# Optimization experiments

Hardware: AMD Instinct MI355X
Metric: run time of the kernel (lower is better)

Reference implementation:

```python
import jax, jax.numpy as jnp
import numpy as np

D_MODEL = 1024
HEADS = 16
D_K = D_MODEL // HEADS
B, S = 4, 2048


def setup_inputs() -> dict:
    key = jax.random.key(0)
    ks = jax.random.split(key, 12)
    xav = float(np.sqrt(6.0 / (D_MODEL + D_MODEL)))  # xavier_uniform bound
    inp = {
        "query": jax.random.normal(ks[0], (B, S, D_MODEL), jnp.float32),
        "key": jax.random.normal(ks[1], (B, S, D_MODEL), jnp.float32),
        "value": jax.random.normal(ks[2], (B, S, D_MODEL), jnp.float32),
        # causal mask, broadcast over batch and heads: [1,1,S,S]
        "mask": jnp.tril(jnp.ones((S, S), jnp.int32))[None, None],
        "Wq": jax.random.uniform(ks[3], (D_MODEL, D_MODEL), jnp.float32, -xav, xav),
        "bq": jnp.zeros((D_MODEL,), jnp.float32),
        "Wk": jax.random.uniform(ks[4], (D_MODEL, D_MODEL), jnp.float32, -xav, xav),
        "bk": jnp.zeros((D_MODEL,), jnp.float32),
        "Wv": jax.random.uniform(ks[5], (D_MODEL, D_MODEL), jnp.float32, -xav, xav),
        "bv": jnp.zeros((D_MODEL,), jnp.float32),
        "Wo": jax.random.uniform(ks[6], (D_MODEL, D_MODEL), jnp.float32, -xav, xav),
        "bo": jnp.zeros((D_MODEL,), jnp.float32),
    }
    return inp


def reference(query, key, value, mask, Wq, bq, Wk, bk, Wv, bv, Wo, bo):
    b, s, d = query.shape
    # torch Linear: y = x @ W.T + b, W is [out, in]
    Q = (jnp.einsum("bsd,ed->bse", query, Wq) + bq).reshape(b, s, HEADS, D_K).transpose(0, 2, 1, 3)
    K = (jnp.einsum("bsd,ed->bse", key, Wk) + bk).reshape(b, -1, HEADS, D_K).transpose(0, 2, 1, 3)
    V = (jnp.einsum("bsd,ed->bse", value, Wv) + bv).reshape(b, -1, HEADS, D_K).transpose(0, 2, 1, 3)
    scale = 1.0 / jnp.sqrt(jnp.asarray(D_K, query.dtype))
    scores = jnp.einsum("bhqd,bhkd->bhqk", Q, K) * scale  # [B,H,S,S]
    scores = jnp.where(mask == 0, -jnp.inf, scores)
    attn = jax.nn.softmax(scores, axis=-1)
    attn = jnp.where(jnp.isnan(attn), jnp.zeros_like(attn), attn)  # nan-fix as in source
    out = jnp.einsum("bhqk,bhkd->bhqd", attn, V)
    out = out.transpose(0, 2, 1, 3).reshape(b, s, d)
    return jnp.einsum("bsd,ed->bse", out, Wo) + bo
```

## Files before the change

kernel.cpp:

```cpp
#include <hip/hip_runtime.h>
#include <hip/hip_bf16.h>

#define DM 1024
#define NHEADS 16
#define DKH 64
#define BATCH 4
#define SEQ 2048
#define MROWS (BATCH*SEQ)

typedef __attribute__((ext_vector_type(8))) short bf16x8;
typedef __attribute__((ext_vector_type(4))) short bf16x4;
typedef __attribute__((ext_vector_type(4))) float f32x4;

#if __has_builtin(__builtin_amdgcn_exp2f)
#define EXP2(x) __builtin_amdgcn_exp2f(x)
#else
#define EXP2(x) exp2f(x)
#endif

__device__ __forceinline__ unsigned short f2bf(float f){
  unsigned u = __float_as_uint(f);
  u += 0x7fffu + ((u >> 16) & 1u);
  return (unsigned short)(u >> 16);
}

__device__ __forceinline__ unsigned pk2bf(float lo, float hi){
  union { __hip_bfloat162 h; unsigned u; } c;
  c.h = __float22bfloat162_rn(make_float2(lo, hi));
  return c.u;
}

__device__ __forceinline__ bf16x8 cvtA8(float4 a, float4 b){
  union { unsigned u[4]; bf16x8 v; } r;
  r.u[0] = pk2bf(a.x, a.y);
  r.u[1] = pk2bf(a.z, a.w);
  r.u[2] = pk2bf(b.x, b.y);
  r.u[3] = pk2bf(b.z, b.w);
  return r.v;
}

__device__ __forceinline__ void gload16(const unsigned short* g, unsigned short* l){
  __builtin_amdgcn_global_load_lds((const __attribute__((address_space(1))) void*)g,
                                   (__attribute__((address_space(3))) void*)l, 16, 0, 0);
}

struct ConvArgs { const float* src[4]; unsigned short* dst[4]; };

__global__ __launch_bounds__(256) void conv_w(ConvArgs a){
  const int t = blockIdx.x >> 10;
  const int boff = blockIdx.x & 1023;
  const float* __restrict__ src = a.src[t];
  unsigned short* __restrict__ dst = a.dst[t];
  const int i = (boff * 256 + threadIdx.x) * 4;
  const float4 v = *reinterpret_cast<const float4*>(src + i);
  ushort4 o;
  o.x = f2bf(v.x); o.y = f2bf(v.y); o.z = f2bf(v.z); o.w = f2bf(v.w);
  *reinterpret_cast<ushort4*>(dst + i) = o;
}

template<int MODE, int AFP32>
__global__ __launch_bounds__(256)
void gemm_bt(const void* __restrict__ Av, const unsigned short* __restrict__ Bw,
             const float* __restrict__ bias, void* __restrict__ out, float scale)
{
  const int K = 1024;
  __shared__ short a_sh[128*64];
  __shared__ short b_sh[128*64];
  const int tid  = threadIdx.x;
  const int lane = tid & 63;
  const int wid  = tid >> 6;
  const int wm = wid >> 1, wn = wid & 1;
  const int lin = blockIdx.x;
  const int xcd = lin & 7;
  const int i9  = lin >> 3;
  const int tileM = (8*xcd + (i9 >> 3)) * 128;
  const int tileN = (i9 & 7) * 128;

  f32x4 acc[4][4];
  #pragma unroll
  for (int i = 0; i < 4; i++)
    #pragma unroll
    for (int j = 0; j < 4; j++)
      acc[i][j] = (f32x4){0.f,0.f,0.f,0.f};

  const int lr = lane & 15;
  const int lg = lane >> 4;

  const int r8 = lane >> 3, c8 = lane & 7;
  const int srow = 8*wid + r8;
  const int sgrp = (c8 ^ r8) * 8;

  for (int k0 = 0; k0 < K; k0 += 64){
    bf16x8 ra[4];
    if constexpr (AFP32){
      const float* Af = (const float*)Av;
      #pragma unroll
      for (int i = 0; i < 4; i++){
        int v   = tid + 256*i;
        int row = v >> 3;
        int cg  = v & 7;
        const float4 f0 = *reinterpret_cast<const float4*>(Af + (size_t)(tileM+row)*K + k0 + cg*8);
        const float4 f1 = *reinterpret_cast<const float4*>(Af + (size_t)(tileM+row)*K + k0 + cg*8 + 4);
        ra[i] = cvtA8(f0, f1);
      }
    }
    __syncthreads();
    #pragma unroll
    for (int j = 0; j < 4; j++){
      gload16(Bw + (size_t)(tileN + srow + 32*j)*K + k0 + sgrp,
              (unsigned short*)&b_sh[(8*wid + 32*j)*64]);
    }
    if constexpr (AFP32){
      #pragma unroll
      for (int i = 0; i < 4; i++){
        int v   = tid + 256*i;
        int row = v >> 3;
        int cg  = v & 7;
        *reinterpret_cast<bf16x8*>(&a_sh[row*64 + ((cg ^ (row & 7)) * 8)]) = ra[i];
      }
    } else {
      const unsigned short* Ab = (const unsigned short*)Av;
      #pragma unroll
      for (int j = 0; j < 4; j++){
        gload16(Ab + (size_t)(tileM + srow + 32*j)*K + k0 + sgrp,
                (unsigned short*)&a_sh[(8*wid + 32*j)*64]);
      }
    }
    __syncthreads();

    #pragma unroll
    for (int kk = 0; kk < 64; kk += 32){
      bf16x8 af[4], bfr[4];
      const int g0 = lg + (kk >> 3);
      #pragma unroll
      for (int fm = 0; fm < 4; fm++){
        int row = wm*64 + fm*16 + lr;
        af[fm] = *reinterpret_cast<const bf16x8*>(&a_sh[row*64 + ((g0 ^ (row & 7)) * 8)]);
      }
      #pragma unroll
      for (int fn = 0; fn < 4; fn++){
        int row = wn*64 + fn*16 + lr;
        bfr[fn] = *reinterpret_cast<const bf16x8*>(&b_sh[row*64 + ((g0 ^ (row & 7)) * 8)]);
      }
      #pragma unroll
      for (int fm = 0; fm < 4; fm++)
        #pragma unroll
        for (int fn = 0; fn < 4; fn++)
          acc[fm][fn] = __builtin_amdgcn_mfma_f32_16x16x32_bf16(af[fm], bfr[fn], acc[fm][fn], 0, 0, 0);
    }
  }

  #pragma unroll
  for (int fm = 0; fm < 4; fm++){
    #pragma unroll
    for (int fn = 0; fn < 4; fn++){
      #pragma unroll
      for (int r = 0; r < 4; r++){
        int m = tileM + wm*64 + fm*16 + lg*4 + r;
        int n = tileN + wn*64 + fn*16 + lr;
        float val = acc[fm][fn][r] + bias[n];
        if (MODE == 0){
          val *= scale;
          int b = m >> 11, s = m & 2047, h = n >> 6, d = n & 63;
          ((unsigned short*)out)[(((size_t)(b*NHEADS + h)*SEQ + s)*DKH + d)] = f2bf(val);
        } else if (MODE == 1){
          int b = m >> 11, s = m & 2047, h = n >> 6, d = n & 63;
          ((unsigned short*)out)[(((size_t)(b*NHEADS + h)*DKH + d)*SEQ + s)] = f2bf(val);
        } else {
          ((float*)out)[(size_t)m*DM + n] = val;
        }
      }
    }
  }
}

__global__ __launch_bounds__(256, 4)
void attn_kernel(const unsigned short* __restrict__ Q, const unsigned short* __restrict__ Kb,
                 const unsigned short* __restrict__ Vt, unsigned short* __restrict__ Oout)
{
  __shared__ unsigned short k_sh[2][64*64];
  __shared__ unsigned short v_sh[2][64*64];
  const int lane = threadIdx.x & 63;
  const int w    = threadIdx.x >> 6;
  const int lr = lane & 15, grp = lane >> 4;
  const int bh = blockIdx.x;
  const int qtile = 15 - (int)blockIdx.y;
  const int qb0 = qtile * 128;
  const int qw0 = qb0 + w * 32;
  const int b = bh >> 4, h = bh & 15;
  const size_t kbase = (size_t)bh * SEQ * DKH;
  const size_t vbase = (size_t)bh * DKH * SEQ;

  const int r8 = lane >> 3, c8 = lane & 7;
  const int rowS0 = w*16 + r8;
  const int rowS1 = w*16 + 8 + r8;
  const size_t offK0 = (size_t)rowS0*DKH  + (size_t)((c8 ^ (rowS0 & 7)) * 8);
  const size_t offK1 = (size_t)rowS1*DKH  + (size_t)((c8 ^ (rowS1 & 7)) * 8);
  const size_t offV0 = (size_t)rowS0*SEQ  + (size_t)((c8 ^ (rowS0 & 7)) * 8);
  const size_t offV1 = (size_t)rowS1*SEQ  + (size_t)((c8 ^ (rowS1 & 7)) * 8);
  const int ldsA = (w*16)*64;
  const int ldsB = (w*16+8)*64;

  bf16x8 qf[2][2];
  #pragma unroll
  for (int qg = 0; qg < 2; qg++){
    size_t off = kbase + (size_t)(qw0 + qg*16 + lr)*DKH + grp*8;
    qf[qg][0] = *reinterpret_cast<const bf16x8*>(Q + off);
    qf[qg][1] = *reinterpret_cast<const bf16x8*>(Q + off + 32);
  }

  bf16x4 ones4;
  ones4[0] = (short)0x3F80; ones4[1] = (short)0x3F80;
  ones4[2] = (short)0x3F80; ones4[3] = (short)0x3F80;

  float mrun[2] = {-__builtin_inff(), -__builtin_inff()};
  f32x4 ls[2];
  f32x4 o[2][4];
  #pragma unroll
  for (int qg = 0; qg < 2; qg++){
    ls[qg] = (f32x4){0.f,0.f,0.f,0.f};
    #pragma unroll
    for (int dc = 0; dc < 4; dc++) o[qg][dc] = (f32x4){0.f,0.f,0.f,0.f};
  }

  const int nkb = qb0/64 + 2;

#define STAGE(kb_, bf_) do { \
    gload16(Kb + kbase + (size_t)(kb_)*4096 + offK0, (unsigned short*)&k_sh[bf_][ldsA]); \
    gload16(Kb + kbase + (size_t)(kb_)*4096 + offK1, (unsigned short*)&k_sh[bf_][ldsB]); \
    gload16(Vt + vbase + (size_t)(kb_)*64   + offV0, (unsigned short*)&v_sh[bf_][ldsA]); \
    gload16(Vt + vbase + (size_t)(kb_)*64   + offV1, (unsigned short*)&v_sh[bf_][ldsB]); \
  } while(0)

  STAGE(0, 0);
  __syncthreads();

  for (int kb = 0; kb < nkb; kb++){
    const int buf = kb & 1;
    if (kb + 1 < nkb) STAGE(kb + 1, buf ^ 1);

    if (kb*64 <= qw0 + 31){
      const unsigned short* ks = k_sh[buf];
      const unsigned short* vs = v_sh[buf];
      const bool act0 = (kb*64 <= qw0 + 15);

      bf16x4 pb[2][4];
      #pragma unroll
      for (int qg = 0; qg < 2; qg++){
        if (qg == 0 && !act0) continue;
        f32x4 st[4];
        __builtin_amdgcn_s_setprio(1);
        #pragma unroll
        for (int ksub = 0; ksub < 4; ksub++){
          int rowk = ksub*16 + lr;
          bf16x8 kf0 = *reinterpret_cast<const bf16x8*>(&ks[rowk*64 + ((grp ^ (rowk & 7)) * 8)]);
          bf16x8 kf1 = *reinterpret_cast<const bf16x8*>(&ks[rowk*64 + (((4 + grp) ^ (rowk & 7)) * 8)]);
          f32x4 s = (f32x4){0.f,0.f,0.f,0.f};
          s = __builtin_amdgcn_mfma_f32_16x16x32_bf16(kf0, qf[qg][0], s, 0, 0, 0);
          s = __builtin_amdgcn_mfma_f32_16x16x32_bf16(kf1, qf[qg][1], s, 0, 0, 0);
          st[ksub] = s;
        }
        __builtin_amdgcn_s_setprio(0);

        const int qgb = qw0 + qg*16;
        if (kb*64 + 63 > qgb){
          #pragma unroll
          for (int ksub = 0; ksub < 4; ksub++)
            #pragma unroll
            for (int r = 0; r < 4; r++){
              int kg = kb*64 + ksub*16 + grp*4 + r;
              if (kg > qgb + lr) st[ksub][r] = -__builtin_inff();
            }
        }
        float mt = fmaxf(fmaxf(st[0][0], st[0][1]), fmaxf(st[0][2], st[0][3]));
        #pragma unroll
        for (int ksub = 1; ksub < 4; ksub++){
          mt = fmaxf(mt, fmaxf(fmaxf(st[ksub][0], st[ksub][1]),
                               fmaxf(st[ksub][2], st[ksub][3])));
        }
        mt = fmaxf(mt, __shfl_xor(mt, 16));
        mt = fmaxf(mt, __shfl_xor(mt, 32));
        const float mnew = fmaxf(mrun[qg], mt);
        const float corr = EXP2(mrun[qg] - mnew);
        mrun[qg] = mnew;
        #pragma unroll
        for (int dc = 0; dc < 4; dc++){
          o[qg][dc][0] *= corr; o[qg][dc][1] *= corr;
          o[qg][dc][2] *= corr; o[qg][dc][3] *= corr;
        }
        ls[qg][0] *= corr;
        #pragma unroll
        for (int ksub = 0; ksub < 4; ksub++){
          float p0 = EXP2(st[ksub][0] - mnew);
          float p1 = EXP2(st[ksub][1] - mnew);
          float p2 = EXP2(st[ksub][2] - mnew);
          float p3 = EXP2(st[ksub][3] - mnew);
          union { unsigned u[2]; bf16x4 v; } pk;
          pk.u[0] = pk2bf(p0, p1);
          pk.u[1] = pk2bf(p2, p3);
          pb[qg][ksub] = pk.v;
        }
      }

      __builtin_amdgcn_s_setprio(1);
      #pragma unroll
      for (int ksub = 0; ksub < 4; ksub++){
        #pragma unroll
        for (int dc = 0; dc < 4; dc++){
          int rowd = dc*16 + lr;
          int cg16 = ksub*2 + (grp >> 1);
          bf16x4 vf = *reinterpret_cast<const bf16x4*>(
              &vs[rowd*64 + ((cg16 ^ (rowd & 7)) * 8) + (grp & 1)*4]);
          if (act0) o[0][dc] = __builtin_amdgcn_mfma_f32_16x16x16bf16_1k(vf, pb[0][ksub], o[0][dc], 0, 0, 0);
          o[1][dc] = __builtin_amdgcn_mfma_f32_16x16x16bf16_1k(vf, pb[1][ksub], o[1][dc], 0, 0, 0);
        }
        if (act0) ls[0] = __builtin_amdgcn_mfma_f32_16x16x16bf16_1k(ones4, pb[0][ksub], ls[0], 0, 0, 0);
        ls[1] = __builtin_amdgcn_mfma_f32_16x16x16bf16_1k(ones4, pb[1][ksub], ls[1], 0, 0, 0);
      }
      __builtin_amdgcn_s_setprio(0);
    }
    __syncthreads();
  }
#undef STAGE

  #pragma unroll
  for (int qg = 0; qg < 2; qg++){
    float inv = 1.0f / ls[qg][0];
    int qglob = qw0 + qg*16 + lr;
    size_t ob = ((size_t)(b*SEQ + qglob))*DM + h*DKH;
    #pragma unroll
    for (int dc = 0; dc < 4; dc++){
      ushort4 pk;
      pk.x = f2bf(o[qg][dc][0]*inv);
      pk.y = f2bf(o[qg][dc][1]*inv);
      pk.z = f2bf(o[qg][dc][2]*inv);
      pk.w = f2bf(o[qg][dc][3]*inv);
      *reinterpret_cast<ushort4*>(&Oout[ob + dc*16 + grp*4]) = pk;
    }
  }
}

extern "C" void kernel_launch(void* const* d_in, const int* in_sizes, int n_in,
                              void* d_out, int out_size, void* d_ws, size_t ws_size,
                              hipStream_t stream) {
  const float* query = (const float*)d_in[0];
  const float* key   = (const float*)d_in[1];
  const float* value = (const float*)d_in[2];
  const float* Wq = (const float*)d_in[4];
  const float* bq = (const float*)d_in[5];
  const float* Wk = (const float*)d_in[6];
  const float* bk = (const float*)d_in[7];
  const float* Wv = (const float*)d_in[8];
  const float* bv = (const float*)d_in[9];
  const float* Wo = (const float*)d_in[10];
  const float* bo = (const float*)d_in[11];
  float* out = (float*)d_out;

  char* ws = (char*)d_ws;
  const size_t SZ_X = (size_t)MROWS * DM * 2;
  const size_t SZ_W = (size_t)DM * DM * 2;
  unsigned short* wqb = (unsigned short*)(ws + 0);
  unsigned short* wkb = (unsigned short*)(ws + SZ_W);
  unsigned short* wvb = (unsigned short*)(ws + 2*SZ_W);
  unsigned short* wob = (unsigned short*)(ws + 3*SZ_W);
  unsigned short* Qb   = (unsigned short*)(ws + 4*SZ_W);
  unsigned short* Kbuf = (unsigned short*)(ws + 4*SZ_W + SZ_X);
  unsigned short* Vt   = (unsigned short*)(ws + 4*SZ_W + 2*SZ_X);
  unsigned short* attO = (unsigned short*)(ws + 4*SZ_W + 3*SZ_X);

  ConvArgs ca;
  ca.src[0] = Wq; ca.src[1] = Wk; ca.src[2] = Wv; ca.src[3] = Wo;
  ca.dst[0] = wqb; ca.dst[1] = wkb; ca.dst[2] = wvb; ca.dst[3] = wob;
  conv_w<<<4096, 256, 0, stream>>>(ca);

  const int NBLK = (MROWS/128) * (DM/128);
  const float qscale = 0.125f * 1.4426950408889634f;
  gemm_bt<1,1><<<NBLK, 256, 0, stream>>>(value, wvb, bv, (void*)Vt,   1.0f);
  gemm_bt<0,1><<<NBLK, 256, 0, stream>>>(query, wqb, bq, (void*)Qb,   qscale);
  gemm_bt<0,1><<<NBLK, 256, 0, stream>>>(key,   wkb, bk, (void*)Kbuf, 1.0f);

  attn_kernel<<<dim3(64, 16), 256, 0, stream>>>(Qb, Kbuf, Vt, attO);

  gemm_bt<2,0><<<NBLK, 256, 0, stream>>>(attO, wob, bo, (void*)out, 1.0f);
}
```

Baseline: 198.6 us.

## Batch Q/K/V projections into one launch and rebalance causal attention tile order

The three separate projection GEMM launches become one grid of 1536 blocks that selects its input, weight, bias and output layout per block, removing two launches and the tail idle time between them. The output projection becomes its own specialized kernel with the bf16 A path only. The attention kernel's query-tile mapping changes from strictly descending order to an interleaved order that mixes heavy and light causal tiles, to even out load across CUs. This adds a runtime branch on the block index in the epilogue.

```diff
diff --git a/kernel.cpp b/kernel.cpp
--- a/kernel.cpp
+++ b/kernel.cpp
@@ -58,10 +58,123 @@
   *reinterpret_cast<ushort4*>(dst + i) = o;
 }
 
-template<int MODE, int AFP32>
+struct QKVArgs {
+  const float* A[3];
+  const unsigned short* W[3];
+  const float* bias[3];
+  unsigned short* out[3];
+  float scale[3];
+};
+
 __global__ __launch_bounds__(256)
-void gemm_bt(const void* __restrict__ Av, const unsigned short* __restrict__ Bw,
-             const float* __restrict__ bias, void* __restrict__ out, float scale)
+void gemm_qkv(QKVArgs args)
+{
+  const int K = 1024;
+  __shared__ short a_sh[128*64];
+  __shared__ short b_sh[128*64];
+  const int tid  = threadIdx.x;
+  const int lane = tid & 63;
+  const int wid  = tid >> 6;
+  const int wm = wid >> 1, wn = wid & 1;
+  const int z   = blockIdx.x >> 9;
+  const int lin = blockIdx.x & 511;
+  const int xcd = lin & 7;
+  const int i9  = lin >> 3;
+  const int tileM = (8*xcd + (i9 >> 3)) * 128;
+  const int tileN = (i9 & 7) * 128;
+
+  const float* __restrict__ Af = args.A[z];
+  const unsigned short* __restrict__ Bw = args.W[z];
+  const float* __restrict__ bias = args.bias[z];
+  unsigned short* __restrict__ outp = args.out[z];
+  const float scale = args.scale[z];
+
+  f32x4 acc[4][4];
+  #pragma unroll
+  for (int i = 0; i < 4; i++)
+    #pragma unroll
+    for (int j = 0; j < 4; j++)
+      acc[i][j] = (f32x4){0.f,0.f,0.f,0.f};
+
+  const int lr = lane & 15;
+  const int lg = lane >> 4;
+
+  const int r8 = lane >> 3, c8 = lane & 7;
+  const int srow = 8*wid + r8;
+  const int sgrp = (c8 ^ r8) * 8;
+
+  for (int k0 = 0; k0 < K; k0 += 64){
+    bf16x8 ra[4];
+    #pragma unroll
+    for (int i = 0; i < 4; i++){
+      int v   = tid + 256*i;
+      int row = v >> 3;
+      int cg  = v & 7;
+      const float4 f0 = *reinterpret_cast<const float4*>(Af + (size_t)(tileM+row)*K + k0 + cg*8);
+      const float4 f1 = *reinterpret_cast<const float4*>(Af + (size_t)(tileM+row)*K + k0 + cg*8 + 4);
+      ra[i] = cvtA8(f0, f1);
+    }
+    __syncthreads();
+    #pragma unroll
+    for (int j = 0; j < 4; j++){
+      gload16(Bw + (size_t)(tileN + srow + 32*j)*K + k0 + sgrp,
+              (unsigned short*)&b_sh[(8*wid + 32*j)*64]);
+    }
+    #pragma unroll
+    for (int i = 0; i < 4; i++){
+      int v   = tid + 256*i;
+      int row = v >> 3;
+      int cg  = v & 7;
+      *reinterpret_cast<bf16x8*>(&a_sh[row*64 + ((cg ^ (row & 7)) * 8)]) = ra[i];
+    }
+    __syncthreads();
+
+    #pragma unroll
+    for (int kk = 0; kk < 64; kk += 32){
+      bf16x8 af[4], bfr[4];
+      const int g0 = lg + (kk >> 3);
+      #pragma unroll
+      for (int fm = 0; fm < 4; fm++){
+        int row = wm*64 + fm*16 + lr;
+        af[fm] = *reinterpret_cast<const bf16x8*>(&a_sh[row*64 + ((g0 ^ (row & 7)) * 8)]);
+      }
+      #pragma unroll
+      for (int fn = 0; fn < 4; fn++){
+        int row = wn*64 + fn*16 + lr;
+        bfr[fn] = *reinterpret_cast<const bf16x8*>(&b_sh[row*64 + ((g0 ^ (row & 7)) * 8)]);
+      }
+      #pragma unroll
+      for (int fm = 0; fm < 4; fm++)
+        #pragma unroll
+        for (int fn = 0; fn < 4; fn++)
+          acc[fm][fn] = __builtin_amdgcn_mfma_f32_16x16x32_bf16(af[fm], bfr[fn], acc[fm][fn], 0, 0, 0);
+    }
+  }
+
+  #pragma unroll
+  for (int fm = 0; fm < 4; fm++){
+    #pragma unroll
+    for (int fn = 0; fn < 4; fn++){
+      #pragma unroll
+      for (int r = 0; r < 4; r++){
+        int m = tileM + wm*64 + fm*16 + lg*4 + r;
+        int n = tileN + wn*64 + fn*16 + lr;
+        float val = acc[fm][fn][r] + bias[n];
+        int b = m >> 11, s = m & 2047, h = n >> 6, d = n & 63;
+        if (z == 0){
+          outp[(((size_t)(b*NHEADS + h)*DKH + d)*SEQ + s)] = f2bf(val);
+        } else {
+          val *= scale;
+          outp[(((size_t)(b*NHEADS + h)*SEQ + s)*DKH + d)] = f2bf(val);
+        }
+      }
+    }
+  }
+}
+
+__global__ __launch_bounds__(256)
+void gemm_out(const unsigned short* __restrict__ Ab, const unsigned short* __restrict__ Bw,
+              const float* __restrict__ bias, float* __restrict__ out)
 {
   const int K = 1024;
   __shared__ short a_sh[128*64];
@@ -85,46 +198,18 @@
 
   const int lr = lane & 15;
   const int lg = lane >> 4;
-
   const int r8 = lane >> 3, c8 = lane & 7;
   const int srow = 8*wid + r8;
   const int sgrp = (c8 ^ r8) * 8;
 
   for (int k0 = 0; k0 < K; k0 += 64){
-    bf16x8 ra[4];
-    if constexpr (AFP32){
-      const float* Af = (const float*)Av;
-      #pragma unroll
-      for (int i = 0; i < 4; i++){
-        int v   = tid + 256*i;
-        int row = v >> 3;
-        int cg  = v & 7;
-        const float4 f0 = *reinterpret_cast<const float4*>(Af + (size_t)(tileM+row)*K + k0 + cg*8);
-        const float4 f1 = *reinterpret_cast<const float4*>(Af + (size_t)(tileM+row)*K + k0 + cg*8 + 4);
-        ra[i] = cvtA8(f0, f1);
-      }
-    }
     __syncthreads();
     #pragma unroll
     for (int j = 0; j < 4; j++){
       gload16(Bw + (size_t)(tileN + srow + 32*j)*K + k0 + sgrp,
               (unsigned short*)&b_sh[(8*wid + 32*j)*64]);
-    }
-    if constexpr (AFP32){
-      #pragma unroll
-      for (int i = 0; i < 4; i++){
-        int v   = tid + 256*i;
-        int row = v >> 3;
-        int cg  = v & 7;
-        *reinterpret_cast<bf16x8*>(&a_sh[row*64 + ((cg ^ (row & 7)) * 8)]) = ra[i];
-      }
-    } else {
-      const unsigned short* Ab = (const unsigned short*)Av;
-      #pragma unroll
-      for (int j = 0; j < 4; j++){
-        gload16(Ab + (size_t)(tileM + srow + 32*j)*K + k0 + sgrp,
-                (unsigned short*)&a_sh[(8*wid + 32*j)*64]);
-      }
+      gload16(Ab + (size_t)(tileM + srow + 32*j)*K + k0 + sgrp,
+              (unsigned short*)&a_sh[(8*wid + 32*j)*64]);
     }
     __syncthreads();
 
@@ -158,17 +243,7 @@
       for (int r = 0; r < 4; r++){
         int m = tileM + wm*64 + fm*16 + lg*4 + r;
         int n = tileN + wn*64 + fn*16 + lr;
-        float val = acc[fm][fn][r] + bias[n];
-        if (MODE == 0){
-          val *= scale;
-          int b = m >> 11, s = m & 2047, h = n >> 6, d = n & 63;
-          ((unsigned short*)out)[(((size_t)(b*NHEADS + h)*SEQ + s)*DKH + d)] = f2bf(val);
-        } else if (MODE == 1){
-          int b = m >> 11, s = m & 2047, h = n >> 6, d = n & 63;
-          ((unsigned short*)out)[(((size_t)(b*NHEADS + h)*DKH + d)*SEQ + s)] = f2bf(val);
-        } else {
-          ((float*)out)[(size_t)m*DM + n] = val;
-        }
+        out[(size_t)m*DM + n] = acc[fm][fn][r] + bias[n];
       }
     }
   }
@@ -184,7 +259,9 @@
   const int w    = threadIdx.x >> 6;
   const int lr = lane & 15, grp = lane >> 4;
   const int bh = blockIdx.x;
-  const int qtile = 15 - (int)blockIdx.y;
+  const int qy = (int)blockIdx.y;
+  const int qg2 = qy >> 2, qr = qy & 3;
+  const int qtile = (qg2 & 1) ? (8 - 8*(qg2 >> 1) + qr) : (15 - 8*(qg2 >> 1) - qr);
   const int qb0 = qtile * 128;
   const int qw0 = qb0 + w * 32;
   const int b = bh >> 4, h = bh & 15;
@@ -373,13 +450,16 @@
   ca.dst[0] = wqb; ca.dst[1] = wkb; ca.dst[2] = wvb; ca.dst[3] = wob;
   conv_w<<<4096, 256, 0, stream>>>(ca);
 
-  const int NBLK = (MROWS/128) * (DM/128);
   const float qscale = 0.125f * 1.4426950408889634f;
-  gemm_bt<1,1><<<NBLK, 256, 0, stream>>>(value, wvb, bv, (void*)Vt,   1.0f);
-  gemm_bt<0,1><<<NBLK, 256, 0, stream>>>(query, wqb, bq, (void*)Qb,   qscale);
-  gemm_bt<0,1><<<NBLK, 256, 0, stream>>>(key,   wkb, bk, (void*)Kbuf, 1.0f);
+  QKVArgs qa;
+  qa.A[0] = value; qa.A[1] = query; qa.A[2] = key;
+  qa.W[0] = wvb;   qa.W[1] = wqb;   qa.W[2] = wkb;
+  qa.bias[0] = bv; qa.bias[1] = bq; qa.bias[2] = bk;
+  qa.out[0] = Vt;  qa.out[1] = Qb;  qa.out[2] = Kbuf;
+  qa.scale[0] = 1.0f; qa.scale[1] = qscale; qa.scale[2] = 1.0f;
+  gemm_qkv<<<1536, 256, 0, stream>>>(qa);
 
   attn_kernel<<<dim3(64, 16), 256, 0, stream>>>(Qb, Kbuf, Vt, attO);
 
-  gemm_bt<2,0><<<NBLK, 256, 0, stream>>>(attO, wob, bo, (void*)out, 1.0f);
-}
+  gemm_out<<<512, 256, 0, stream>>>(attO, wob, bo, out);
+}
```

Result: slower. 202.5 us (+2.0%).
